# Kernel tuning notes

Measured on AMD Instinct MI355X. Metric: run time of the kernel, lower is better.

## Reference

```python
import jax, jax.numpy as jnp
import numpy as np

N, DX, DS, NLAB, NSMAT = 20000, 16, 64, 10, 64
E_HALF = 160000
E = 2 * E_HALF
N_LABELED = 2000
N_HIDDEN = 6  # six Linear(nsmat,nsmat) layers between input and output layers


def setup_inputs() -> dict:
    key = jax.random.key(0)
    ks = jax.random.split(key, 16)
    xembed = jax.random.normal(ks[0], (N, DX), jnp.float32)
    sembed = jax.random.normal(ks[1], (N, DS), jnp.float32)
    # ylprob are log-probabilities (original uses exp(ylprob) in the KL term)
    ylprob = jax.nn.log_softmax(jax.random.normal(ks[2], (N, NLAB), jnp.float32), axis=1)
    # build edge list with explicit reverse pairs so loss_orth is exercised
    s_half = jax.random.randint(ks[3], (E_HALF,), 0, N, jnp.int32)
    t_half = jax.random.randint(ks[4], (E_HALF,), 0, N, jnp.int32)
    src = jnp.concatenate([s_half, t_half])
    tgt = jnp.concatenate([t_half, s_half])
    edge_w = jax.random.uniform(ks[5], (E,), jnp.float32, 0.1, 1.0)
    rev1 = jnp.arange(E_HALF, dtype=jnp.int32)
    rev2 = rev1 + E_HALF
    idvert = jax.random.randint(ks[6], (N_LABELED,), 0, N, jnp.int32)
    fcW_in = jax.random.normal(ks[7], (2 * DS, NSMAT), jnp.float32) / np.sqrt(2 * DS)
    fcb_in = jnp.zeros((NSMAT,), jnp.float32)
    fcW_h = jax.random.normal(ks[8], (N_HIDDEN, NSMAT, NSMAT), jnp.float32) / np.sqrt(NSMAT)
    fcb_h = jnp.zeros((N_HIDDEN, NSMAT), jnp.float32)
    fcW_out = jax.random.normal(ks[9], (NSMAT, DX * DX), jnp.float32) / np.sqrt(NSMAT)
    fcb_out = jnp.zeros((DX * DX,), jnp.float32)
    # cl_smat params: Linear(dimx, nlab) + LogSoftmax
    clW = jax.random.normal(ks[10], (DX, NLAB), jnp.float32) / np.sqrt(DX)
    clb = jnp.zeros((NLAB,), jnp.float32)
    return dict(xembed=xembed, sembed=sembed, ylprob=ylprob, edge_w=edge_w,
                fcW_in=fcW_in, fcb_in=fcb_in, fcW_h=fcW_h, fcb_h=fcb_h,
                fcW_out=fcW_out, fcb_out=fcb_out, clW=clW, clb=clb,
                src=src, tgt=tgt, rev1=rev1, rev2=rev2, idvert=idvert)


def _edge_matrices(sf, tf, fcW_in, fcb_in, fcW_h, fcb_h, fcW_out, fcb_out):
    # [E, 2*dims] -> 8-layer ReLU MLP -> [E, dimx, dimx]
    h = jax.nn.relu(jnp.concatenate([sf, tf], axis=1) @ fcW_in + fcb_in)
    for i in range(N_HIDDEN):
        h = jax.nn.relu(h @ fcW_h[i] + fcb_h[i])
    return (h @ fcW_out + fcb_out).reshape(-1, DX, DX)


def reference(xembed, sembed, ylprob, edge_w, fcW_in, fcb_in, fcW_h, fcb_h,
              fcW_out, fcb_out, clW, clb, src, tgt, rev1, rev2, idvert):
    # per-edge sheaf transport matrices from gathered structure embeddings
    edge_mats = _edge_matrices(sembed[src], sembed[tgt],
                               fcW_in, fcb_in, fcW_h, fcb_h, fcW_out, fcb_out)

    # orthogonality loss over reverse edge pairs: mean RMS(A@B - I) * dimx
    prod = jnp.einsum('eij,ejk->eik', edge_mats[rev1], edge_mats[rev2])
    diff = prod - jnp.eye(DX, dtype=prod.dtype)
    loss_orth = jnp.mean(jnp.sqrt(jnp.mean(diff * diff, axis=(1, 2)) * (DX * DX)))

    # message passing: gather -> bmm -> weighted scatter-add -> degree normalize
    messages = jnp.einsum('eij,ej->ei', edge_mats, xembed[src])  # [E, dimx]
    weighted = messages * edge_w[:, None]
    new_x = jax.ops.segment_sum(weighted, tgt, num_segments=N)   # [N, dimx]
    deg = jax.ops.segment_sum(edge_w, tgt, num_segments=N)       # [N]
    xmaped = jnp.where((deg > 0)[:, None], new_x / jnp.maximum(deg, 1e-20)[:, None], new_x)

    loss_smap = jnp.mean((xmaped - xembed) ** 2) * DX

    # KL(y || g) on labeled nodes; cl_smat = Linear + LogSoftmax
    glprob = jax.nn.log_softmax(xmaped[idvert] @ clW + clb, axis=1)
    ylp = ylprob[idvert]
    loss_lbpr = jnp.mean(jnp.sum(jnp.exp(ylp) * (ylp - glprob), axis=1))

    # original recomputes the same MLP on the same inputs and takes the MSE of
    # two identical tensors -> exactly zero (and zero gradient)
    loss_cons = jnp.zeros((), xembed.dtype)

    return (loss_orth, loss_cons, loss_smap, loss_lbpr)
```

## Files before the change

kernel.cpp:

```cpp
#include <hip/hip_runtime.h>
#include <hip/hip_bf16.h>

#define N_NODES   20000
#define DX        16
#define DS        64
#define NLAB      10
#define NSMAT     64
#define E_HALF    160000
#define E_TOT     320000
#define N_LABELED 2000
#define N_HIDDEN  6

#define PAIRS 32
#define NT    (E_HALF / PAIRS)

typedef short bf16x8 __attribute__((ext_vector_type(8)));
typedef float f32x4  __attribute__((ext_vector_type(4)));
#define MFMA16(a, b, c) __builtin_amdgcn_mfma_f32_16x16x32_bf16((a), (b), (c), 0, 0, 0)

#define LDS_A0    0
#define LDS_H0    16384
#define LDS_H1    24576
#define LDS_MT    24576
#define LDS_TOTAL 40960

#define SWZ(row)  ((((row) & 7) << 4) ^ (((row) & 8) << 2))
#define CSP(c)    (((c) & 12) << 2)

#define WS_W0     0
#define WS_WH     16384
#define WS_WOUT   65536
#define WS_FLOATS 98304

__device__ __forceinline__ unsigned short f2bf(float f) {
    unsigned int u = __float_as_uint(f);
    unsigned int r = (u + 0x7fffu + ((u >> 16) & 1u)) >> 16;
    return (unsigned short)r;
}
__device__ __forceinline__ unsigned int cvtpk(float lo, float hi) {
    unsigned int r;
    asm("v_cvt_pk_bf16_f32 %0, %1, %2" : "=v"(r) : "v"(lo), "v"(hi));
    return r;
}
__device__ __forceinline__ float bflo(unsigned int u) { return __uint_as_float(u << 16); }
__device__ __forceinline__ float bfhi(unsigned int u) { return __uint_as_float(u & 0xffff0000u); }

__global__ void k_prep(const float* __restrict__ Win, const float* __restrict__ Wh,
                       const float* __restrict__ Wout, unsigned short* __restrict__ wsw) {
    const int idx = blockIdx.x * 256 + threadIdx.x;
    if (idx >= 49152) return;
    float val; int base, KK, k, n;
    if (idx < 8192) {
        k = idx >> 6; n = idx & 63; val = Win[idx]; base = WS_W0 / 2; KK = 4;
    } else if (idx < 32768) {
        const int r = idx - 8192; const int l = r >> 12; const int rr = r & 4095;
        k = rr >> 6; n = rr & 63; val = Wh[r]; base = (WS_WH + l * 8192) / 2; KK = 2;
    } else {
        const int r = idx - 32768; k = r >> 8; n = r & 255;
        val = Wout[r]; base = WS_WOUT / 2; KK = 2;
    }
    const int ntile = n >> 4, kk = k >> 5, hi = (k >> 3) & 3, j = k & 7;
    const int lane = hi * 16 + (n & 15);
    wsw[base + (((ntile * KK + kk) * 64 + lane) * 8 + j)] = f2bf(val);
}

__global__ void k_zero(float* __restrict__ p, int n) {
    int i = blockIdx.x * blockDim.x + threadIdx.x;
    const int stride = gridDim.x * blockDim.x;
    for (; i < n; i += stride) p[i] = 0.0f;
}

__global__ __launch_bounds__(256, 4) void k_main(
    const float* __restrict__ xembed, const float* __restrict__ sembed,
    const float* __restrict__ edge_w,
    const float* __restrict__ bin, const float* __restrict__ bh,
    const float* __restrict__ bout,
    const int* __restrict__ src, const int* __restrict__ tgt,
    const unsigned short* __restrict__ wsw,
    float* __restrict__ newx, float* __restrict__ deg,
    float* __restrict__ orth_part)
{
    extern __shared__ char lds[];
    const int tid    = threadIdx.x;
    const int lane   = tid & 63;
    const int wv     = tid >> 6;
    const int lane15 = lane & 15;
    const int hi     = lane >> 4;
    const int p0     = blockIdx.x * PAIRS;

    float4 sx;
    {
        const int si = tid >> 3, sc = tid & 7;
        const bool sT = (sc >= 4); const int scc = sc & 3;
        const int p = p0 + si;
        const int nodeA = sT ? tgt[p] : src[p];
        const float4* nrow = (const float4*)(sembed + (size_t)nodeA * DS + scc * 16);
        const float4 v0 = nrow[0], v1 = nrow[1], v2 = nrow[2], v3 = nrow[3];
        const int colA = (sT ? 128 : 0) + scc * 32;
        const int colB = (sT ? 0 : 128) + scc * 32;
        const int sXor = SWZ(si);
        uint2 pk;
        pk.x = cvtpk(v0.x, v0.y); pk.y = cvtpk(v0.z, v0.w);
        *(uint2*)(lds + LDS_A0 + si * 256 + ((colA + 0) ^ sXor)) = pk;
        *(uint2*)(lds + LDS_A0 + (32 + si) * 256 + ((colB + 0) ^ sXor)) = pk;
        pk.x = cvtpk(v1.x, v1.y); pk.y = cvtpk(v1.z, v1.w);
        *(uint2*)(lds + LDS_A0 + si * 256 + ((colA + 8) ^ sXor)) = pk;
        *(uint2*)(lds + LDS_A0 + (32 + si) * 256 + ((colB + 8) ^ sXor)) = pk;
        pk.x = cvtpk(v2.x, v2.y); pk.y = cvtpk(v2.z, v2.w);
        *(uint2*)(lds + LDS_A0 + si * 256 + ((colA + 16) ^ sXor)) = pk;
        *(uint2*)(lds + LDS_A0 + (32 + si) * 256 + ((colB + 16) ^ sXor)) = pk;
        pk.x = cvtpk(v3.x, v3.y); pk.y = cvtpk(v3.z, v3.w);
        *(uint2*)(lds + LDS_A0 + si * 256 + ((colA + 24) ^ sXor)) = pk;
        *(uint2*)(lds + LDS_A0 + (32 + si) * 256 + ((colB + 24) ^ sXor)) = pk;

        const int sed = tid >> 2, sqq = tid & 3;
        const int nodeX = (sed < 32) ? src[p0 + sed] : tgt[p0 + sed - 32];
        sx = *(const float4*)(xembed + (size_t)nodeX * DX + sqq * 4);
    }

    float bin_r[4];
    #pragma unroll
    for (int n = 0; n < 4; ++n) bin_r[n] = bin[16 * n + lane15];

    const int arow = 16 * wv + lane15;
    const int axor = SWZ(arow);

    bf16x8 wcur[8], wnxt[8];
    {
        const unsigned short* whg = wsw + WS_WH / 2;
        #pragma unroll
        for (int j = 0; j < 8; ++j)
            wcur[j] = *(const bf16x8*)(whg + (j * 64 + lane) * 8);
    }

    __syncthreads();

    {
        bf16x8 a[4];
        #pragma unroll
        for (int kk = 0; kk < 4; ++kk)
            a[kk] = *(const bf16x8*)(lds + LDS_A0 + arow * 256 + ((kk * 64 + hi * 16) ^ axor));
        const unsigned short* w0g = wsw + WS_W0 / 2;
        #pragma unroll
        for (int n = 0; n < 4; ++n) {
            f32x4 acc = {0.0f, 0.0f, 0.0f, 0.0f};
            #pragma unroll
            for (int kk = 0; kk < 4; ++kk) {
                const bf16x8 b = *(const bf16x8*)(w0g + ((n * 4 + kk) * 64 + lane) * 8);
                acc = MFMA16(a[kk], b, acc);
            }
            #pragma unroll
            for (int r = 0; r < 4; ++r) {
                const int row = 16 * wv + 4 * hi + r;
                *(__hip_bfloat16*)(lds + LDS_H0 + row * 128 +
                    (((16 * n + lane15) * 2) ^ SWZ(row))) =
                    __float2bfloat16(fmaxf(acc[r] + bin_r[n], 0.0f));
            }
        }
    }

    float bcur[4], bnxt[4];
    {
        const float* bl = bh + lane15;
        bcur[0] = bl[0]; bcur[1] = bl[16]; bcur[2] = bl[32]; bcur[3] = bl[48];
    }
    #pragma unroll
    for (int l = 0; l < N_HIDDEN; ++l) {
        if (l + 1 < N_HIDDEN) {
            const unsigned short* whg = wsw + WS_WH / 2 + (l + 1) * 4096;
            #pragma unroll
            for (int j = 0; j < 8; ++j)
                wnxt[j] = *(const bf16x8*)(whg + (j * 64 + lane) * 8);
            const float* bl = bh + (l + 1) * 64 + lane15;
            bnxt[0] = bl[0]; bnxt[1] = bl[16]; bnxt[2] = bl[32]; bnxt[3] = bl[48];
        }
        const int sB = (l & 1) ? LDS_H1 : LDS_H0;
        const int dB = (l & 1) ? LDS_H0 : LDS_H1;
        const bf16x8 a0 = *(const bf16x8*)(lds + sB + arow * 128 + ((hi * 16) ^ axor));
        const bf16x8 a1 = *(const bf16x8*)(lds + sB + arow * 128 + ((64 + hi * 16) ^ axor));
        #pragma unroll
        for (int n = 0; n < 4; ++n) {
            f32x4 acc = {0.0f, 0.0f, 0.0f, 0.0f};
            acc = MFMA16(a0, wcur[2 * n + 0], acc);
            acc = MFMA16(a1, wcur[2 * n + 1], acc);
            #pragma unroll
            for (int r = 0; r < 4; ++r) {
                const int row = 16 * wv + 4 * hi + r;
                *(__hip_bfloat16*)(lds + dB + row * 128 +
                    (((16 * n + lane15) * 2) ^ SWZ(row))) =
                    __float2bfloat16(fmaxf(acc[r] + bcur[n], 0.0f));
            }
        }
        #pragma unroll
        for (int j = 0; j < 8; ++j) wcur[j] = wnxt[j];
        bcur[0] = bnxt[0]; bcur[1] = bnxt[1]; bcur[2] = bnxt[2]; bcur[3] = bnxt[3];
    }
    __syncthreads();

    {
        float bo[16];
        #pragma unroll
        for (int n = 0; n < 16; ++n) bo[n] = bout[16 * n + lane15];

        const bf16x8 fa0 = *(const bf16x8*)(lds + LDS_H0 + arow * 128 + ((hi * 16) ^ axor));
        const bf16x8 fa1 = *(const bf16x8*)(lds + LDS_H0 + arow * 128 + ((64 + hi * 16) ^ axor));
        const unsigned short* wog = wsw + WS_WOUT / 2;

        bf16x8 pbA[4], pbB[4];
        #pragma unroll
        for (int n = 0; n < 4; ++n) {
            pbA[n] = *(const bf16x8*)(wog + ((n * 2 + 0) * 64 + lane) * 8);
            pbB[n] = *(const bf16x8*)(wog + ((n * 2 + 1) * 64 + lane) * 8);
        }

        if (wv < 2) {
            #pragma unroll
            for (int n = 0; n < 16; ++n) {
                const bf16x8 b0 = pbA[n & 3], b1 = pbB[n & 3];
                if (n + 4 < 16) {
                    pbA[n & 3] = *(const bf16x8*)(wog + (((n + 4) * 2 + 0) * 64 + lane) * 8);
                    pbB[n & 3] = *(const bf16x8*)(wog + (((n + 4) * 2 + 1) * 64 + lane) * 8);
                }
                f32x4 acc = {0.0f, 0.0f, 0.0f, 0.0f};
                acc = MFMA16(fa0, b0, acc);
                acc = MFMA16(fa1, b1, acc);
                #pragma unroll
                for (int r = 0; r < 4; ++r) {
                    const int i = 16 * wv + 4 * hi + r;
                    *(__hip_bfloat16*)(lds + LDS_A0 + i * 512 +
                        (((n * 16 + lane15) * 2) ^ SWZ(i))) =
                        __float2bfloat16(acc[r] + bo[n]);
                }
            }
        } else {
            unsigned int pk0[8], pk1[8], pk2[8], pk3[8];
            float tmp0 = 0.f, tmp1 = 0.f, tmp2 = 0.f, tmp3 = 0.f;
            #pragma unroll
            for (int n = 0; n < 16; ++n) {
                const bf16x8 b0 = pbA[n & 3], b1 = pbB[n & 3];
                if (n + 4 < 16) {
                    pbA[n & 3] = *(const bf16x8*)(wog + (((n + 4) * 2 + 0) * 64 + lane) * 8);
                    pbB[n & 3] = *(const bf16x8*)(wog + (((n + 4) * 2 + 1) * 64 + lane) * 8);
                }
                f32x4 acc = {0.0f, 0.0f, 0.0f, 0.0f};
                acc = MFMA16(fa0, b0, acc);
                acc = MFMA16(fa1, b1, acc);
                const float v0 = acc[0] + bo[n], v1 = acc[1] + bo[n];
                const float v2 = acc[2] + bo[n], v3 = acc[3] + bo[n];
                if (n & 1) {
                    pk0[n >> 1] = cvtpk(tmp0, v0); pk1[n >> 1] = cvtpk(tmp1, v1);
                    pk2[n >> 1] = cvtpk(tmp2, v2); pk3[n >> 1] = cvtpk(tmp3, v3);
                } else {
                    tmp0 = v0; tmp1 = v1; tmp2 = v2; tmp3 = v3;
                }
            }
            const int csp = CSP(lane15);
            #pragma unroll
            for (int r = 0; r < 4; ++r) {
                const int i = 16 * (wv - 2) + 4 * hi + r;
                const int sw = SWZ(i) ^ csp;
                char* base = lds + LDS_MT + i * 512;
                const unsigned int* pkr = (r == 0) ? pk0 : (r == 1) ? pk1 : (r == 2) ? pk2 : pk3;
                *(uint4*)(base + ((lane15 * 32 + 0) ^ sw)) =
                    make_uint4(pkr[0], pkr[1], pkr[2], pkr[3]);
                *(uint4*)(base + ((lane15 * 32 + 16) ^ sw)) =
                    make_uint4(pkr[4], pkr[5], pkr[6], pkr[7]);
            }
        }
    }
    __syncthreads();

    {
        const int e = tid >> 2, q = tid & 3;
        const int i = e & 31;
        const bool isB = (e >= 32);
        float xv[16];
        #pragma unroll
        for (int qq = 0; qq < 4; ++qq) {
            xv[4 * qq + 0] = __shfl(sx.x, qq, 4);
            xv[4 * qq + 1] = __shfl(sx.y, qq, 4);
            xv[4 * qq + 2] = __shfl(sx.z, qq, 4);
            xv[4 * qq + 3] = __shfl(sx.w, qq, 4);
        }
        const int p = p0 + i;
        const float w_e  = isB ? edge_w[p + E_HALF] : edge_w[p];
        const int target = isB ? src[p] : tgt[p];
        const int ixor = SWZ(i);
        if (!isB) {
            #pragma unroll
            for (int jj = 0; jj < 4; ++jj) {
                const int row = 4 * q + jj;
                const uint4 m0 = *(const uint4*)(lds + LDS_A0 + i * 512 + ((row * 32) ^ ixor));
                const uint4 m1 = *(const uint4*)(lds + LDS_A0 + i * 512 + ((row * 32 + 16) ^ ixor));
                float m = bflo(m0.x) * xv[0];
                m = fmaf(bfhi(m0.x), xv[1], m);  m = fmaf(bflo(m0.y), xv[2], m);
                m = fmaf(bfhi(m0.y), xv[3], m);  m = fmaf(bflo(m0.z), xv[4], m);
                m = fmaf(bfhi(m0.z), xv[5], m);  m = fmaf(bflo(m0.w), xv[6], m);
                m = fmaf(bfhi(m0.w), xv[7], m);  m = fmaf(bflo(m1.x), xv[8], m);
                m = fmaf(bfhi(m1.x), xv[9], m);  m = fmaf(bflo(m1.y), xv[10], m);
                m = fmaf(bfhi(m1.y), xv[11], m); m = fmaf(bflo(m1.z), xv[12], m);
                m = fmaf(bfhi(m1.z), xv[13], m); m = fmaf(bflo(m1.w), xv[14], m);
                m = fmaf(bfhi(m1.w), xv[15], m);
                atomicAdd(&newx[(size_t)target * DX + row], w_e * m);
            }
        } else {
            float macc[4] = {0.f, 0.f, 0.f, 0.f};
            #pragma unroll
            for (int c = 0; c < 16; ++c) {
                const uint2 v = *(const uint2*)(lds + LDS_MT + i * 512 +
                                                ((c * 32 + q * 8) ^ ixor ^ CSP(c)));
                const float xc = xv[c];
                macc[0] = fmaf(bflo(v.x), xc, macc[0]);
                macc[1] = fmaf(bfhi(v.x), xc, macc[1]);
                macc[2] = fmaf(bflo(v.y), xc, macc[2]);
                macc[3] = fmaf(bfhi(v.y), xc, macc[3]);
            }
            #pragma unroll
            for (int jj = 0; jj < 4; ++jj)
                atomicAdd(&newx[(size_t)target * DX + 4 * q + jj], w_e * macc[jj]);
        }
        if (q == 0) atomicAdd(&deg[target], w_e);
    }

    float wsum = 0.0f;
    {
        const bf16x8 zf = {0, 0, 0, 0, 0, 0, 0, 0};
        #pragma unroll
        for (int pp = 0; pp < 8; ++pp) {
            const int pi = 8 * wv + pp;
            const int pxor = SWZ(pi);
            const int offA = (lane15 * 32 + (hi & 1) * 16) ^ pxor;
            const int offB = (lane15 * 32 + (hi & 1) * 16) ^ pxor ^ CSP(lane15);
            bf16x8 af  = *(const bf16x8*)(lds + LDS_A0 + pi * 512 + offA);
            bf16x8 bfr = *(const bf16x8*)(lds + LDS_MT + pi * 512 + offB);
            if (hi >= 2) { af = zf; bfr = zf; }
            f32x4 pr = {0.f, 0.f, 0.f, 0.f};
            pr = MFMA16(af, bfr, pr);
            float ss = 0.0f;
            #pragma unroll
            for (int r = 0; r < 4; ++r) {
                const float d = pr[r] - ((4 * hi + r == lane15) ? 1.0f : 0.0f);
                ss = fmaf(d, d, ss);
            }
            #pragma unroll
            for (int o = 32; o > 0; o >>= 1) ss += __shfl_xor(ss, o, 64);
            wsum += sqrtf(ss);
        }
    }
    __syncthreads();
    if (lane == 0) ((float*)(lds + LDS_A0))[wv] = wsum;
    __syncthreads();
    if (tid == 0) {
        const float* pw = (const float*)(lds + LDS_A0);
        atomicAdd(&orth_part[blockIdx.x & 255], pw[0] + pw[1] + pw[2] + pw[3]);
    }
}

__device__ __forceinline__ float block_reduce_256(float v) {
    __shared__ float part[4];
    #pragma unroll
    for (int off = 32; off > 0; off >>= 1) v += __shfl_xor(v, off, 64);
    const int lane = threadIdx.x & 63, wid = threadIdx.x >> 6;
    if (lane == 0) part[wid] = v;
    __syncthreads();
    float s = 0.0f;
    if (threadIdx.x == 0) {
        #pragma unroll
        for (int i = 0; i < 4; ++i) s += part[i];
    }
    return s;
}

__global__ __launch_bounds__(256) void k_smap(
    const float* __restrict__ xembed, float* __restrict__ nx,
    const float* __restrict__ deg, float* __restrict__ accum)
{
    const int n = blockIdx.x * 256 + threadIdx.x;
    float ss = 0.0f;
    if (n < N_NODES) {
        const float d = deg[n];
        const float inv = 1.0f / fmaxf(d, 1e-20f);
        #pragma unroll
        for (int c = 0; c < DX; ++c) {
            const float v  = nx[(size_t)n * DX + c];
            const float xm = (d > 0.0f) ? v * inv : v;
            nx[(size_t)n * DX + c] = xm;
            const float df = xm - xembed[(size_t)n * DX + c];
            ss = fmaf(df, df, ss);
        }
    }
    ss = block_reduce_256(ss);
    if (threadIdx.x == 0) atomicAdd(&accum[1], ss);
}

__global__ __launch_bounds__(256) void k_lbpr(
    const float* __restrict__ ylprob, const float* __restrict__ xmaped,
    const float* __restrict__ clW, const float* __restrict__ clb,
    const int* __restrict__ idvert, float* __restrict__ accum)
{
    const int v = blockIdx.x * 256 + threadIdx.x;
    float kl = 0.0f;
    if (v < N_LABELED) {
        const int n = idvert[v];
        float z[NLAB];
        #pragma unroll
        for (int c = 0; c < NLAB; ++c) z[c] = clb[c];
        #pragma unroll
        for (int i = 0; i < DX; ++i) {
            const float xi = xmaped[(size_t)n * DX + i];
            #pragma unroll
            for (int c = 0; c < NLAB; ++c) z[c] = fmaf(xi, clW[i * NLAB + c], z[c]);
        }
        float mx = z[0];
        #pragma unroll
        for (int c = 1; c < NLAB; ++c) mx = fmaxf(mx, z[c]);
        float se = 0.0f;
        #pragma unroll
        for (int c = 0; c < NLAB; ++c) se += expf(z[c] - mx);
        const float lse = mx + logf(se);
        #pragma unroll
        for (int c = 0; c < NLAB; ++c) {
            const float yl = ylprob[(size_t)n * NLAB + c];
            kl += expf(yl) * (yl - (z[c] - lse));
        }
    }
    kl = block_reduce_256(kl);
    if (threadIdx.x == 0) atomicAdd(&accum[2], kl);
}

__global__ __launch_bounds__(256) void k_final(
    const float* __restrict__ accum, const float* __restrict__ orth_part,
    float* __restrict__ out)
{
    float v = orth_part[threadIdx.x];
    v = block_reduce_256(v);
    if (threadIdx.x == 0) {
        out[0] = v * (1.0f / (float)E_HALF);
        out[1] = 0.0f;
        out[2] = accum[1] * (1.0f / (float)N_NODES);
        out[3] = accum[2] * (1.0f / (float)N_LABELED);
    }
}

extern "C" void kernel_launch(void* const* d_in, const int* in_sizes, int n_in,
                              void* d_out, int out_size, void* d_ws, size_t ws_size,
                              hipStream_t stream) {
    const float* xembed = (const float*)d_in[0];
    const float* sembed = (const float*)d_in[1];
    const float* ylprob = (const float*)d_in[2];
    const float* edge_w = (const float*)d_in[3];
    const float* Win    = (const float*)d_in[4];
    const float* bin    = (const float*)d_in[5];
    const float* Wh     = (const float*)d_in[6];
    const float* bh     = (const float*)d_in[7];
    const float* Wout   = (const float*)d_in[8];
    const float* bout   = (const float*)d_in[9];
    const float* clW    = (const float*)d_in[10];
    const float* clb    = (const float*)d_in[11];
    const int*   src    = (const int*)d_in[12];
    const int*   tgt    = (const int*)d_in[13];
    const int*   idvert = (const int*)d_in[16];

    unsigned short* wsw = (unsigned short*)d_ws;
    float* wsF       = (float*)((char*)d_ws + WS_FLOATS);
    float* newx      = wsF;
    float* deg       = wsF + (size_t)N_NODES * DX;
    float* accum     = deg + N_NODES;
    float* orth_part = accum + 4;
    const int nzero = N_NODES * DX + N_NODES + 4 + 256;

    k_prep<<<192, 256, 0, stream>>>(Win, Wh, Wout, wsw);
    k_zero<<<512, 256, 0, stream>>>(wsF, nzero);

    k_main<<<NT, 256, LDS_TOTAL, stream>>>(
        xembed, sembed, edge_w, bin, bh, bout, src, tgt, wsw, newx, deg, orth_part);

    k_smap<<<(N_NODES + 255) / 256, 256, 0, stream>>>(xembed, newx, deg, accum);
    k_lbpr<<<(N_LABELED + 255) / 256, 256, 0, stream>>>(ylprob, newx, clW, clb, idvert, accum);
    k_final<<<1, 256, 0, stream>>>(accum, orth_part, (float*)d_out);
}
```

Baseline: 129.6 us.

## Privatize scatter-add into replicated slices and move orth loss before scatter

The node-feature and degree accumulators are replicated into up to 8 slices selected by block index, so the atomics from concurrent blocks are spread over separate copies. k_smap then sums the slices while normalizing. The orth-loss MFMA block is moved ahead of the scatter phase, which drops one barrier and reuses a different LDS region for the partial sums. In exchange it zeroes and reads 8x more accumulator memory and adds a serial reduction over the slices in k_smap.

Result: slower. 162.0 us (+25.0%).

```diff
diff --git a/kernel.cpp b/kernel.cpp
--- a/kernel.cpp
+++ b/kernel.cpp
@@ -77,8 +77,8 @@
     const float* __restrict__ bout,
     const int* __restrict__ src, const int* __restrict__ tgt,
     const unsigned short* __restrict__ wsw,
-    float* __restrict__ newx, float* __restrict__ deg,
-    float* __restrict__ orth_part)
+    float* __restrict__ newxb, float* __restrict__ degb,
+    float* __restrict__ orth_part, int smask)
 {
     extern __shared__ char lds[];
     const int tid    = threadIdx.x;
@@ -87,6 +87,9 @@
     const int lane15 = lane & 15;
     const int hi     = lane >> 4;
     const int p0     = blockIdx.x * PAIRS;
+    const int slice  = blockIdx.x & smask;
+    float* __restrict__ newx = newxb + (size_t)slice * (N_NODES * DX);
+    float* __restrict__ deg  = degb  + (size_t)slice * N_NODES;
 
     float4 sx;
     {
@@ -270,6 +273,38 @@
     }
     __syncthreads();
 
+    float wsum = 0.0f;
+    {
+        const bf16x8 zf = {0, 0, 0, 0, 0, 0, 0, 0};
+        #pragma unroll
+        for (int pp = 0; pp < 8; ++pp) {
+            const int pi = 8 * wv + pp;
+            const int pxor = SWZ(pi);
+            const int offA = (lane15 * 32 + (hi & 1) * 16) ^ pxor;
+            const int offB = (lane15 * 32 + (hi & 1) * 16) ^ pxor ^ CSP(lane15);
+            bf16x8 af  = *(const bf16x8*)(lds + LDS_A0 + pi * 512 + offA);
+            bf16x8 bfr = *(const bf16x8*)(lds + LDS_MT + pi * 512 + offB);
+            if (hi >= 2) { af = zf; bfr = zf; }
+            f32x4 pr = {0.f, 0.f, 0.f, 0.f};
+            pr = MFMA16(af, bfr, pr);
+            float ss = 0.0f;
+            #pragma unroll
+            for (int r = 0; r < 4; ++r) {
+                const float d = pr[r] - ((4 * hi + r == lane15) ? 1.0f : 0.0f);
+                ss = fmaf(d, d, ss);
+            }
+            #pragma unroll
+            for (int o = 32; o > 0; o >>= 1) ss += __shfl_xor(ss, o, 64);
+            wsum += sqrtf(ss);
+        }
+    }
+    if (lane == 0) ((float*)(lds + LDS_H0))[wv] = wsum;
+    __syncthreads();
+    if (tid == 0) {
+        const float* pw = (const float*)(lds + LDS_H0);
+        atomicAdd(&orth_part[blockIdx.x & 255], pw[0] + pw[1] + pw[2] + pw[3]);
+    }
+
     {
         const int e = tid >> 2, q = tid & 3;
         const int i = e & 31;
@@ -321,39 +356,6 @@
         }
         if (q == 0) atomicAdd(&deg[target], w_e);
     }
-
-    float wsum = 0.0f;
-    {
-        const bf16x8 zf = {0, 0, 0, 0, 0, 0, 0, 0};
-        #pragma unroll
-        for (int pp = 0; pp < 8; ++pp) {
-            const int pi = 8 * wv + pp;
-            const int pxor = SWZ(pi);
-            const int offA = (lane15 * 32 + (hi & 1) * 16) ^ pxor;
-            const int offB = (lane15 * 32 + (hi & 1) * 16) ^ pxor ^ CSP(lane15);
-            bf16x8 af  = *(const bf16x8*)(lds + LDS_A0 + pi * 512 + offA);
-            bf16x8 bfr = *(const bf16x8*)(lds + LDS_MT + pi * 512 + offB);
-            if (hi >= 2) { af = zf; bfr = zf; }
-            f32x4 pr = {0.f, 0.f, 0.f, 0.f};
-            pr = MFMA16(af, bfr, pr);
-            float ss = 0.0f;
-            #pragma unroll
-            for (int r = 0; r < 4; ++r) {
-                const float d = pr[r] - ((4 * hi + r == lane15) ? 1.0f : 0.0f);
-                ss = fmaf(d, d, ss);
-            }
-            #pragma unroll
-            for (int o = 32; o > 0; o >>= 1) ss += __shfl_xor(ss, o, 64);
-            wsum += sqrtf(ss);
-        }
-    }
-    __syncthreads();
-    if (lane == 0) ((float*)(lds + LDS_A0))[wv] = wsum;
-    __syncthreads();
-    if (tid == 0) {
-        const float* pw = (const float*)(lds + LDS_A0);
-        atomicAdd(&orth_part[blockIdx.x & 255], pw[0] + pw[1] + pw[2] + pw[3]);
-    }
 }
 
 __device__ __forceinline__ float block_reduce_256(float v) {
@@ -372,19 +374,22 @@
 }
 
 __global__ __launch_bounds__(256) void k_smap(
-    const float* __restrict__ xembed, float* __restrict__ nx,
-    const float* __restrict__ deg, float* __restrict__ accum)
+    const float* __restrict__ xembed, float* __restrict__ nxb,
+    const float* __restrict__ degb, float* __restrict__ accum, int nslice)
 {
     const int n = blockIdx.x * 256 + threadIdx.x;
     float ss = 0.0f;
     if (n < N_NODES) {
-        const float d = deg[n];
+        float d = 0.0f;
+        for (int s = 0; s < nslice; ++s) d += degb[(size_t)s * N_NODES + n];
         const float inv = 1.0f / fmaxf(d, 1e-20f);
         #pragma unroll
         for (int c = 0; c < DX; ++c) {
-            const float v  = nx[(size_t)n * DX + c];
+            float v = 0.0f;
+            for (int s = 0; s < nslice; ++s)
+                v += nxb[(size_t)s * N_NODES * DX + (size_t)n * DX + c];
             const float xm = (d > 0.0f) ? v * inv : v;
-            nx[(size_t)n * DX + c] = xm;
+            nxb[(size_t)n * DX + c] = xm;
             const float df = xm - xembed[(size_t)n * DX + c];
             ss = fmaf(df, df, ss);
         }
@@ -461,21 +466,26 @@
     const int*   tgt    = (const int*)d_in[13];
     const int*   idvert = (const int*)d_in[16];
 
+    const size_t per_slice = (size_t)N_NODES * DX + N_NODES;
+    const size_t need8 = WS_FLOATS + (8 * per_slice + 4 + 256) * sizeof(float);
+    const int nslice = (ws_size >= need8) ? 8 : 1;
+
     unsigned short* wsw = (unsigned short*)d_ws;
     float* wsF       = (float*)((char*)d_ws + WS_FLOATS);
-    float* newx      = wsF;
-    float* deg       = wsF + (size_t)N_NODES * DX;
-    float* accum     = deg + N_NODES;
+    float* newxb     = wsF;
+    float* degb      = wsF + (size_t)nslice * N_NODES * DX;
+    float* accum     = degb + (size_t)nslice * N_NODES;
     float* orth_part = accum + 4;
-    const int nzero = N_NODES * DX + N_NODES + 4 + 256;
+    const int nzero  = (int)((size_t)nslice * per_slice + 4 + 256);
 
     k_prep<<<192, 256, 0, stream>>>(Win, Wh, Wout, wsw);
-    k_zero<<<512, 256, 0, stream>>>(wsF, nzero);
+    k_zero<<<2048, 256, 0, stream>>>(wsF, nzero);
 
     k_main<<<NT, 256, LDS_TOTAL, stream>>>(
-        xembed, sembed, edge_w, bin, bh, bout, src, tgt, wsw, newx, deg, orth_part);
-
-    k_smap<<<(N_NODES + 255) / 256, 256, 0, stream>>>(xembed, newx, deg, accum);
-    k_lbpr<<<(N_LABELED + 255) / 256, 256, 0, stream>>>(ylprob, newx, clW, clb, idvert, accum);
+        xembed, sembed, edge_w, bin, bh, bout, src, tgt, wsw,
+        newxb, degb, orth_part, nslice - 1);
+
+    k_smap<<<(N_NODES + 255) / 256, 256, 0, stream>>>(xembed, newxb, degb, accum, nslice);
+    k_lbpr<<<(N_LABELED + 255) / 256, 256, 0, stream>>>(ylprob, newxb, clW, clb, idvert, accum);
     k_final<<<1, 256, 0, stream>>>(accum, orth_part, (float*)d_out);
 }
```
